# Performance work log

Measured on AMD Instinct MI355X. Metric: run time of the kernel, lower is better.

The kernel has to match this reference:

```python
import jax, jax.numpy as jnp
import numpy as np

EPS = float(np.finfo(np.float64).eps)  # np.finfo(float).eps as in torch combine


def setup_inputs() -> dict:
    key = jax.random.key(0)
    ks = jax.random.split(key, 4)
    B, E, D_in, D_h, D_out = 4096, 8, 768, 2048, 768
    return {
        "x": jax.random.normal(ks[0], (B, D_in), dtype=jnp.float32),
        "w_gate": jax.random.normal(ks[1], (D_in, E), dtype=jnp.float32) * 0.02,
        "W1": jax.random.normal(ks[2], (E, D_in, D_h), dtype=jnp.float32) * (1.0 / np.sqrt(D_in)),
        "b1": jnp.zeros((E, D_h), dtype=jnp.float32),
        "W2": jax.random.normal(ks[3], (E, D_h, D_out), dtype=jnp.float32) * (1.0 / np.sqrt(D_h)),
        "b2": jnp.zeros((E, D_out), dtype=jnp.float32),
        "k": 2,
    }


def _cv_squared(v):
    # torch .var() is unbiased (ddof=1)
    return jnp.var(v, ddof=1) / (jnp.mean(v) ** 2 + 1e-10)


def _top_k_gates(logits, k):
    B, E = logits.shape
    top_vals, top_idx = jax.lax.top_k(logits, k)        # [B, k]
    top_gates = jax.nn.softmax(top_vals, axis=1)        # softmax over the k kept logits
    gates = jnp.zeros((B, E), logits.dtype).at[jnp.arange(B)[:, None], top_idx].set(top_gates)
    return gates


def reference(x, w_gate, W1, b1, W2, b2, k):
    # --- gating (eval path: noiseless clean logits, softmax gating) ---
    logits = x @ w_gate                                  # [B, E]
    gates = _top_k_gates(logits, k)                      # [B, E], sparse (k nonzeros/row)
    # --- per-expert MLP: Linear -> gelu -> Linear -> log_softmax ---
    # Dense grouped compute over experts; gate==0 terms contribute nothing in combine.
    h = jax.nn.gelu(jnp.einsum('bi,eih->beh', x, W1) + b1[None])      # [B, E, Dh]
    lo = jax.nn.log_softmax(jnp.einsum('beh,eho->beo', h, W2) + b2[None], axis=-1)  # [B, E, Do]
    # --- combine: exp, weight by gates, scatter-add, eps-clamp, log ---
    combined = jnp.einsum('be,beo->bo', gates, jnp.exp(lo))           # [B, Do]
    y = jnp.log(jnp.where(combined == 0, EPS, combined))
    # --- load-balancing aux loss (eval: load = count of nonzero gates) ---
    importance = gates.sum(0)
    load = (gates > 0).sum(0).astype(jnp.float32)
    loss = 0.01 * (_cv_squared(importance) + _cv_squared(load))
    return y, loss
```

## Files before the change

### kernel.cpp

```cpp
#include <hip/hip_runtime.h>
#include <hip/hip_bf16.h>
#include <math.h>

typedef __hip_bfloat16 bf16;
typedef short v8s __attribute__((ext_vector_type(8)));
typedef float v4f __attribute__((ext_vector_type(4)));

#define B_TOK 4096
#define E_EXP 8
#define D_IN  768
#define D_H   2048
#define D_OUT 768
#define MAXT  72

__device__ __forceinline__ void gl_lds16(const bf16* g, bf16* l) {
  __builtin_amdgcn_global_load_lds(
      (const __attribute__((address_space(1))) unsigned int*)g,
      (__attribute__((address_space(3))) unsigned int*)l, 16, 0, 0);
}

__global__ void gate_cvt_kernel(const float* __restrict__ x, const float* __restrict__ wg,
                                bf16* __restrict__ xb,
                                float* __restrict__ gates, int* __restrict__ tidx) {
  int gt = blockIdx.x * 256 + threadIdx.x;
  int tok = gt >> 6, l = gt & 63;
  const float* xr = x + (size_t)tok * D_IN;
  bf16* xbr = xb + (size_t)tok * D_IN;
  float acc[8] = {0.f,0.f,0.f,0.f,0.f,0.f,0.f,0.f};
  #pragma unroll
  for (int i = 0; i < 3; ++i) {
    int k0 = i * 256 + l * 4;
    float4 v = *(const float4*)(xr + k0);
    union { bf16 h[4]; uint2 u; } pk;
    pk.h[0] = __float2bfloat16(v.x); pk.h[1] = __float2bfloat16(v.y);
    pk.h[2] = __float2bfloat16(v.z); pk.h[3] = __float2bfloat16(v.w);
    *(uint2*)(xbr + k0) = pk.u;
    float xv[4] = {v.x, v.y, v.z, v.w};
    #pragma unroll
    for (int j = 0; j < 4; ++j) {
      const float* wr = wg + (size_t)(k0 + j) * 8;
      float4 w0 = *(const float4*)wr;
      float4 w1 = *(const float4*)(wr + 4);
      acc[0] += xv[j] * w0.x; acc[1] += xv[j] * w0.y;
      acc[2] += xv[j] * w0.z; acc[3] += xv[j] * w0.w;
      acc[4] += xv[j] * w1.x; acc[5] += xv[j] * w1.y;
      acc[6] += xv[j] * w1.z; acc[7] += xv[j] * w1.w;
    }
  }
  #pragma unroll
  for (int d = 1; d < 64; d <<= 1)
    #pragma unroll
    for (int e = 0; e < 8; ++e) acc[e] += __shfl_xor(acc[e], d);
  if (l == 0) {
    int i1 = 0; float v1 = acc[0];
    #pragma unroll
    for (int e = 1; e < 8; ++e) if (acc[e] > v1) { v1 = acc[e]; i1 = e; }
    int i2 = -1; float v2 = -1e30f;
    #pragma unroll
    for (int e = 0; e < 8; ++e) if (e != i1 && acc[e] > v2) { v2 = acc[e]; i2 = e; }
    float ex = __expf(v2 - v1);
    float g1 = 1.f / (1.f + ex), g2 = ex / (1.f + ex);
    gates[2 * tok] = g1; gates[2 * tok + 1] = g2;
    tidx[2 * tok] = i1;  tidx[2 * tok + 1] = i2;
  }
}

__global__ void finalize_kernel(const int* __restrict__ tidx, const float* __restrict__ gates,
                                int* __restrict__ cnt_off, int* __restrict__ row_ids,
                                int* __restrict__ pos, int* __restrict__ tmap,
                                float* __restrict__ loss_out) {
  __shared__ int   hcnt[256][9];
  __shared__ float himp[256][9];
  __shared__ int   tot[8], off[8];
  __shared__ float itot[8];
  int t = threadIdx.x;
  #pragma unroll
  for (int e = 0; e < 8; ++e) { hcnt[t][e] = 0; himp[t][e] = 0.f; }
  __syncthreads();
  for (int i = 0; i < 32; ++i) {
    int idx = t * 32 + i;
    int e = tidx[idx];
    hcnt[t][e] += 1;
    himp[t][e] += gates[idx];
  }
  __syncthreads();
  if (t < 8) {
    int run = 0; float s = 0.f;
    for (int j = 0; j < 256; ++j) {
      int c = hcnt[j][t];
      hcnt[j][t] = run;
      run += c;
      s += himp[j][t];
    }
    tot[t] = run; itot[t] = s;
  }
  __syncthreads();
  if (t == 0) {
    int o = 0;
    float mi = 0.f, ml = 0.f;
    for (int e = 0; e < 8; ++e) {
      off[e] = o; o += tot[e];
      cnt_off[e] = tot[e]; cnt_off[8 + e] = off[e];
      mi += itot[e]; ml += (float)tot[e];
    }
    mi *= 0.125f; ml *= 0.125f;
    float vi = 0.f, vl = 0.f;
    for (int e = 0; e < 8; ++e) {
      float d = itot[e] - mi;        vi += d * d;
      float d2 = (float)tot[e] - ml; vl += d2 * d2;
    }
    vi /= 7.f; vl /= 7.f;
    *loss_out = 0.01f * (vi / (mi * mi + 1e-10f) + vl / (ml * ml + 1e-10f));
    int nt = 0;
    for (int e = 0; e < 8; ++e)
      for (int tt = 0; tt < (tot[e] + 127) >> 7; ++tt) {
        tmap[nt] = e; tmap[MAXT + nt] = tt; ++nt;
      }
    for (; nt < MAXT; ++nt) tmap[nt] = -1;
  }
  __syncthreads();
  for (int i = 0; i < 32; ++i) {
    int idx = t * 32 + i;
    int e = tidx[idx];
    int slot = off[e] + hcnt[t][e];
    hcnt[t][e] += 1;
    row_ids[slot] = idx >> 1;
    pos[idx] = slot;
  }
}

__global__ void transpose_cvt(const float* __restrict__ W, bf16* __restrict__ Wt,
                              int K, int N) {
  __shared__ bf16 tile[64][72];
  int e = blockIdx.z;
  int k0 = blockIdx.y * 64, n0 = blockIdx.x * 64;
  const float* Wp = W + (size_t)e * K * N;
  bf16* Wtp = Wt + (size_t)e * N * K;
  int t = threadIdx.x;
  int cr = t >> 4;
  int cc = (t & 15) * 4;
  #pragma unroll
  for (int p = 0; p < 4; ++p) {
    int kr = cr + p * 16;
    float4 v = *(const float4*)(Wp + (size_t)(k0 + kr) * N + n0 + cc);
    tile[cc + 0][kr] = __float2bfloat16(v.x);
    tile[cc + 1][kr] = __float2bfloat16(v.y);
    tile[cc + 2][kr] = __float2bfloat16(v.z);
    tile[cc + 3][kr] = __float2bfloat16(v.w);
  }
  __syncthreads();
  #pragma unroll
  for (int p = 0; p < 2; ++p) {
    int o = p * 256 + t;
    int n = o >> 3, k8 = (o & 7) * 8;
    v8s val = *(const v8s*)&tile[n][k8];
    *(v8s*)(Wtp + (size_t)(n0 + n) * K + k0 + k8) = val;
  }
}

template<int KDIM, bool GATHER, bool GELU>
__global__ __launch_bounds__(256, 2)
void gemm_mlp(const bf16* __restrict__ Ab, const bf16* __restrict__ Wt,
              const float* __restrict__ bias, bf16* __restrict__ Outb,
              const int* __restrict__ row_ids, const int* __restrict__ cnt_off,
              const int* __restrict__ tmap, const int N) {
  constexpr int BK = 64, BM = 128, BN = 128;
  constexpr int NK = KDIM / BK;
  static_assert(NK % 2 == 0 && NK >= 4, "NK even, >=4");
  __shared__ __align__(16) bf16 lds[2][(BM + BN) * BK];
  const int ti = blockIdx.y;
  const int e = tmap[ti];
  if (e < 0) return;
  const int rowb = tmap[MAXT + ti];
  const int cnt = cnt_off[e];
  const int off = cnt_off[8 + e];
  const int colb = blockIdx.x;
  const int t = (int)threadIdx.x, w = t >> 6, l = t & 63;
  const int cs = (l & 7) ^ (l >> 3);
  const bf16* gA[4];
  const bf16* gB[4];
  #pragma unroll
  for (int it = 0; it < 4; ++it) {
    int rt = (it * 4 + w) * 8 + (l >> 3);
    int r = rowb * BM + rt;
    int rc = r < cnt ? r : cnt - 1;
    long arow = GATHER ? (long)row_ids[off + rc] : (long)(off + rc);
    gA[it] = Ab + arow * (long)KDIM + cs * 8;
  }
  #pragma unroll
  for (int it = 0; it < 4; ++it) {
    int rt = (it * 4 + w) * 8 + (l >> 3);
    gB[it] = Wt + ((size_t)e * N + (size_t)colb * BN + rt) * KDIM + cs * 8;
  }
  v4f acc[4][4] = {};
  const int wm = w >> 1, wn = w & 1;

#define STAGE(b, k0) do {                                                   \
    _Pragma("unroll")                                                       \
    for (int it = 0; it < 4; ++it)                                          \
      gl_lds16(gA[it] + (k0), &lds[b][(it * 4 + w) * 512]);                 \
    _Pragma("unroll")                                                       \
    for (int it = 0; it < 4; ++it)                                          \
      gl_lds16(gB[it] + (k0), &lds[b][BM * BK + (it * 4 + w) * 512]);       \
  } while (0)

#define COMPUTE(b) do {                                                     \
    __builtin_amdgcn_s_setprio(1);                                          \
    _Pragma("unroll")                                                       \
    for (int kk = 0; kk < 2; ++kk) {                                        \
      v8s af[4], bfr[4];                                                    \
      _Pragma("unroll")                                                     \
      for (int fm = 0; fm < 4; ++fm) {                                      \
        int row = wm * 64 + fm * 16 + (l & 15);                             \
        int cg = kk * 4 + (l >> 4);                                         \
        af[fm] = *(const v8s*)(&lds[b][0] + row * BK + ((cg ^ (row & 7)) << 3)); \
      }                                                                     \
      _Pragma("unroll")                                                     \
      for (int fn = 0; fn < 4; ++fn) {                                      \
        int row = wn * 64 + fn * 16 + (l & 15);                             \
        int cg = kk * 4 + (l >> 4);                                         \
        bfr[fn] = *(const v8s*)(&lds[b][BM * BK] + row * BK + ((cg ^ (row & 7)) << 3)); \
      }                                                                     \
      _Pragma("unroll")                                                     \
      for (int fm = 0; fm < 4; ++fm)                                        \
        _Pragma("unroll")                                                   \
        for (int fn = 0; fn < 4; ++fn)                                      \
          acc[fm][fn] = __builtin_amdgcn_mfma_f32_16x16x32_bf16(af[fm], bfr[fn], acc[fm][fn], 0, 0, 0); \
    }                                                                       \
    __builtin_amdgcn_s_setprio(0);                                          \
  } while (0)

#define SB    __builtin_amdgcn_sched_barrier(0)
#define BARR  __builtin_amdgcn_s_barrier()
#define WAIT8 asm volatile("s_waitcnt vmcnt(8)" ::: "memory")
#define WAITZ asm volatile("s_waitcnt vmcnt(0)" ::: "memory")

  STAGE(0, 0);
  #pragma unroll 1
  for (int ks = 0; ks < NK - 2; ks += 2) {
    STAGE(1, (ks + 1) * BK);
    WAIT8; SB; BARR; SB;
    COMPUTE(0);
    BARR; SB;
    STAGE(0, (ks + 2) * BK);
    WAIT8; SB; BARR; SB;
    COMPUTE(1);
    BARR; SB;
  }
  STAGE(1, (NK - 1) * BK);
  WAIT8; SB; BARR; SB;
  COMPUTE(0);
  WAITZ; SB; BARR; SB;
  COMPUTE(1);
#undef STAGE
#undef COMPUTE
#undef WAIT8
#undef WAITZ

  float* eps = (float*)(&lds[0][0]) + w * (16 * 68);
  const float* bp = bias + (size_t)e * N + (size_t)colb * BN + wn * 64 + (l & 7) * 8;
  float bv[8];
  #pragma unroll
  for (int jj = 0; jj < 8; ++jj) bv[jj] = bp[jj];
  #pragma unroll
  for (int fm = 0; fm < 4; ++fm) {
    #pragma unroll
    for (int fn = 0; fn < 4; ++fn)
      #pragma unroll
      for (int q = 0; q < 4; ++q)
        eps[((l >> 4) * 4 + q) * 68 + fn * 16 + (l & 15)] = acc[fm][fn][q];
    #pragma unroll
    for (int half = 0; half < 2; ++half) {
      int row = (l >> 3) + 8 * half;
      int r = rowb * BM + wm * 64 + fm * 16 + row;
      if (r < cnt) {
        const float* rp = eps + row * 68 + (l & 7) * 8;
        union { bf16 h[8]; uint4 u; } pk;
        #pragma unroll
        for (int jj = 0; jj < 8; ++jj) {
          float v = rp[jj] + bv[jj];
          if (GELU) {
            float u = 0.7978845608028654f * (v + 0.044715f * v * v * v);
            float th = 1.f - 2.f / (__expf(2.f * u) + 1.f);
            v = 0.5f * v * (1.f + th);
          }
          pk.h[jj] = __float2bfloat16(v);
        }
        *(uint4*)(Outb + (size_t)(off + r) * N + (size_t)colb * BN + wn * 64 + (l & 7) * 8) = pk.u;
      }
    }
  }
#undef SB
#undef BARR
}

__global__ void combine_kernel(const bf16* __restrict__ z, const float* __restrict__ gates,
                               const int* __restrict__ pos, float* __restrict__ y) {
  int gt = blockIdx.x * 256 + threadIdx.x;
  int tok = gt >> 6, l = gt & 63;
  if (tok >= B_TOK) return;
  const bf16* z1 = z + (size_t)pos[2 * tok] * D_OUT;
  const bf16* z2 = z + (size_t)pos[2 * tok + 1] * D_OUT;
  float g1 = gates[2 * tok], g2 = gates[2 * tok + 1];
  float a[12], b[12];
  float m1 = -1e30f, m2 = -1e30f;
  #pragma unroll
  for (int i = 0; i < 12; ++i) {
    a[i] = __bfloat162float(z1[l + 64 * i]);
    b[i] = __bfloat162float(z2[l + 64 * i]);
    m1 = fmaxf(m1, a[i]); m2 = fmaxf(m2, b[i]);
  }
  #pragma unroll
  for (int d = 1; d < 64; d <<= 1) {
    m1 = fmaxf(m1, __shfl_xor(m1, d));
    m2 = fmaxf(m2, __shfl_xor(m2, d));
  }
  float s1 = 0.f, s2 = 0.f;
  #pragma unroll
  for (int i = 0; i < 12; ++i) { s1 += __expf(a[i] - m1); s2 += __expf(b[i] - m2); }
  #pragma unroll
  for (int d = 1; d < 64; d <<= 1) { s1 += __shfl_xor(s1, d); s2 += __shfl_xor(s2, d); }
  float c1 = g1 / s1, c2 = g2 / s2;
  #pragma unroll
  for (int i = 0; i < 12; ++i) {
    float cmb = c1 * __expf(a[i] - m1) + c2 * __expf(b[i] - m2);
    y[(size_t)tok * D_OUT + l + 64 * i] = logf(cmb == 0.f ? 2.2204460492503131e-16f : cmb);
  }
}

extern "C" void kernel_launch(void* const* d_in, const int* in_sizes, int n_in,
                              void* d_out, int out_size, void* d_ws, size_t ws_size,
                              hipStream_t stream) {
  const float* x  = (const float*)d_in[0];
  const float* wg = (const float*)d_in[1];
  const float* W1 = (const float*)d_in[2];
  const float* b1 = (const float*)d_in[3];
  const float* W2 = (const float*)d_in[4];
  const float* b2 = (const float*)d_in[5];
  float* out = (float*)d_out;

  char* ws = (char*)d_ws;
  int*   cnt_off = (int*)(ws + 0);
  float* gates   = (float*)(ws + 256);
  int*   tidx    = (int*)(ws + 256 + 32768);
  int*   pos     = (int*)(ws + 256 + 65536);
  int*   row_ids = (int*)(ws + 256 + 98304);
  int*   tmap    = (int*)(ws + 256 + 131072);
  const size_t base = 262144;
  bf16* x_bf = (bf16*)(ws + base);
  bf16* W1t  = (bf16*)(ws + base + 6291456);
  bf16* W2t  = (bf16*)(ws + base + 31457280);
  bf16* h_bf = (bf16*)(ws + base + 56623104);
  bf16* z_bf = (bf16*)(ws + base);

  transpose_cvt<<<dim3(D_H / 64,  D_IN / 64, E_EXP), 256, 0, stream>>>(W1, W1t, D_IN, D_H);
  transpose_cvt<<<dim3(D_OUT / 64, D_H / 64, E_EXP), 256, 0, stream>>>(W2, W2t, D_H, D_OUT);
  gate_cvt_kernel<<<dim3(1024), 256, 0, stream>>>(x, wg, x_bf, gates, tidx);
  finalize_kernel<<<dim3(1), 256, 0, stream>>>(tidx, gates, cnt_off, row_ids, pos, tmap,
                                               out + (size_t)B_TOK * D_OUT);
  gemm_mlp<D_IN, true,  true ><<<dim3(D_H / 128,  MAXT), 256, 0, stream>>>(
      x_bf, W1t, b1, h_bf, row_ids, cnt_off, tmap, D_H);
  gemm_mlp<D_H,  false, false><<<dim3(D_OUT / 128, MAXT), 256, 0, stream>>>(
      h_bf, W2t, b2, z_bf, row_ids, cnt_off, tmap, D_OUT);
  combine_kernel<<<dim3(1024), 256, 0, stream>>>(z_bf, gates, pos, out);
}
```

Before: 162.5 us.

## Use 256x256 GEMM tiles with 8 waves and interleaved staging in expert MLP

The grouped expert GEMMs move from 128x128 tiles with 4 waves to 256x256 tiles with 8 waves (512 threads), which halves the number of row tiles per expert and changes how the tile map is built. The K-loop now issues next-tile global-to-LDS loads partway through the MFMA work, splitting A and B staging across sub-steps, and waits on LDS reads explicitly. The second GEMM swaps its grid axes so row tiles vary fastest. Larger tiles raise data reuse per block, but they also produce fewer blocks (more idle CUs) and more padded rows for small expert groups, and they increase register and LDS pressure.

Result: no change. 164.5 us (+1.2%).

```diff
diff --git a/kernel.cpp b/kernel.cpp
--- a/kernel.cpp
+++ b/kernel.cpp
@@ -11,7 +11,7 @@
 #define D_IN  768
 #define D_H   2048
 #define D_OUT 768
-#define MAXT  72
+#define MAXT  40
 
 __device__ __forceinline__ void gl_lds16(const bf16* g, bf16* l) {
   __builtin_amdgcn_global_load_lds(
@@ -113,7 +113,7 @@
     *loss_out = 0.01f * (vi / (mi * mi + 1e-10f) + vl / (ml * ml + 1e-10f));
     int nt = 0;
     for (int e = 0; e < 8; ++e)
-      for (int tt = 0; tt < (tot[e] + 127) >> 7; ++tt) {
+      for (int tt = 0; tt < (tot[e] + 255) >> 8; ++tt) {
         tmap[nt] = e; tmap[MAXT + nt] = tt; ++nt;
       }
     for (; nt < MAXT; ++nt) tmap[nt] = -1;
@@ -158,112 +158,136 @@
   }
 }
 
-template<int KDIM, bool GATHER, bool GELU>
-__global__ __launch_bounds__(256, 2)
+template<int KDIM, bool GATHER, bool GELU, bool COLX>
+__global__ __launch_bounds__(512, 2)
 void gemm_mlp(const bf16* __restrict__ Ab, const bf16* __restrict__ Wt,
               const float* __restrict__ bias, bf16* __restrict__ Outb,
               const int* __restrict__ row_ids, const int* __restrict__ cnt_off,
               const int* __restrict__ tmap, const int N) {
-  constexpr int BK = 64, BM = 128, BN = 128;
+  constexpr int BK = 64, BM = 256, BN = 256;
   constexpr int NK = KDIM / BK;
   static_assert(NK % 2 == 0 && NK >= 4, "NK even, >=4");
   __shared__ __align__(16) bf16 lds[2][(BM + BN) * BK];
-  const int ti = blockIdx.y;
+  const int cb = COLX ? blockIdx.x : blockIdx.y;
+  const int ti = COLX ? blockIdx.y : blockIdx.x;
   const int e = tmap[ti];
   if (e < 0) return;
   const int rowb = tmap[MAXT + ti];
   const int cnt = cnt_off[e];
   const int off = cnt_off[8 + e];
-  const int colb = blockIdx.x;
   const int t = (int)threadIdx.x, w = t >> 6, l = t & 63;
   const int cs = (l & 7) ^ (l >> 3);
   const bf16* gA[4];
   const bf16* gB[4];
   #pragma unroll
   for (int it = 0; it < 4; ++it) {
-    int rt = (it * 4 + w) * 8 + (l >> 3);
+    int rt = (it * 8 + w) * 8 + (l >> 3);
     int r = rowb * BM + rt;
     int rc = r < cnt ? r : cnt - 1;
     long arow = GATHER ? (long)row_ids[off + rc] : (long)(off + rc);
     gA[it] = Ab + arow * (long)KDIM + cs * 8;
-  }
-  #pragma unroll
-  for (int it = 0; it < 4; ++it) {
-    int rt = (it * 4 + w) * 8 + (l >> 3);
-    gB[it] = Wt + ((size_t)e * N + (size_t)colb * BN + rt) * KDIM + cs * 8;
-  }
-  v4f acc[4][4] = {};
-  const int wm = w >> 1, wn = w & 1;
-
-#define STAGE(b, k0) do {                                                   \
+    gB[it] = Wt + ((size_t)e * N + (size_t)cb * BN + rt) * KDIM + cs * 8;
+  }
+  v4f acc[8][4] = {};
+  const int wm = w >> 2, wn = w & 3;
+
+#define STAGE_A(b, k0) do {                                                 \
     _Pragma("unroll")                                                       \
     for (int it = 0; it < 4; ++it)                                          \
-      gl_lds16(gA[it] + (k0), &lds[b][(it * 4 + w) * 512]);                 \
+      gl_lds16(gA[it] + (k0), &lds[b][(it * 8 + w) * 512]);                 \
+  } while (0)
+#define STAGE_B(b, k0) do {                                                 \
     _Pragma("unroll")                                                       \
     for (int it = 0; it < 4; ++it)                                          \
-      gl_lds16(gB[it] + (k0), &lds[b][BM * BK + (it * 4 + w) * 512]);       \
+      gl_lds16(gB[it] + (k0), &lds[b][BM * BK + (it * 8 + w) * 512]);       \
   } while (0)
 
-#define COMPUTE(b) do {                                                     \
-    __builtin_amdgcn_s_setprio(1);                                          \
+#define READ_A(b, fm, kk) (*(const v8s*)(&lds[b][0] +                       \
+    (wm * 128 + (fm) * 16 + (l & 15)) * 64 +                                \
+    ((((kk) * 4 + (l >> 4)) ^ (l & 7)) << 3)))
+#define READ_B(b, fn, kk) (*(const v8s*)(&lds[b][BM * BK] +                 \
+    (wn * 64 + (fn) * 16 + (l & 15)) * 64 +                                 \
+    ((((kk) * 4 + (l >> 4)) ^ (l & 7)) << 3)))
+
+#define SB    __builtin_amdgcn_sched_barrier(0)
+#define BARR  __builtin_amdgcn_s_barrier()
+#define LGKM0 asm volatile("s_waitcnt lgkmcnt(0)" ::: "memory")
+#define VM0   asm volatile("s_waitcnt vmcnt(0)" ::: "memory")
+
+#define MFMA8(fmb, fm2)                                                     \
     _Pragma("unroll")                                                       \
-    for (int kk = 0; kk < 2; ++kk) {                                        \
-      v8s af[4], bfr[4];                                                    \
+    for (int fn = 0; fn < 4; ++fn)                                          \
       _Pragma("unroll")                                                     \
-      for (int fm = 0; fm < 4; ++fm) {                                      \
-        int row = wm * 64 + fm * 16 + (l & 15);                             \
-        int cg = kk * 4 + (l >> 4);                                         \
-        af[fm] = *(const v8s*)(&lds[b][0] + row * BK + ((cg ^ (row & 7)) << 3)); \
-      }                                                                     \
+      for (int kk = 0; kk < 2; ++kk)                                        \
+        acc[(fmb) + (fm2)][fn] = __builtin_amdgcn_mfma_f32_16x16x32_bf16(   \
+            af[fm2][kk], bfr[fn][kk], acc[(fmb) + (fm2)][fn], 0, 0, 0);
+
+#define TILE(b, nb, knext) do {                                             \
+    v8s bfr[4][2];                                                          \
+    {                              \
+      v8s af[2][2];                                                         \
       _Pragma("unroll")                                                     \
       for (int fn = 0; fn < 4; ++fn) {                                      \
-        int row = wn * 64 + fn * 16 + (l & 15);                             \
-        int cg = kk * 4 + (l >> 4);                                         \
-        bfr[fn] = *(const v8s*)(&lds[b][BM * BK] + row * BK + ((cg ^ (row & 7)) << 3)); \
+        bfr[fn][0] = READ_B(b, fn, 0); bfr[fn][1] = READ_B(b, fn, 1);       \
       }                                                                     \
-      _Pragma("unroll")                                                     \
-      for (int fm = 0; fm < 4; ++fm)                                        \
-        _Pragma("unroll")                                                   \
-        for (int fn = 0; fn < 4; ++fn)                                      \
-          acc[fm][fn] = __builtin_amdgcn_mfma_f32_16x16x32_bf16(af[fm], bfr[fn], acc[fm][fn], 0, 0, 0); \
+      af[0][0] = READ_A(b, 0, 0); af[0][1] = READ_A(b, 0, 1);               \
+      af[1][0] = READ_A(b, 1, 0); af[1][1] = READ_A(b, 1, 1);               \
+      if ((knext) < KDIM) STAGE_A(nb, knext);                               \
+      LGKM0; SB;                                                            \
+      __builtin_amdgcn_s_setprio(1); MFMA8(0, 0) MFMA8(0, 1)                \
+      __builtin_amdgcn_s_setprio(0);                                        \
     }                                                                       \
-    __builtin_amdgcn_s_setprio(0);                                          \
+    {                                        \
+      v8s af[2][2];                                                         \
+      af[0][0] = READ_A(b, 2, 0); af[0][1] = READ_A(b, 2, 1);               \
+      af[1][0] = READ_A(b, 3, 0); af[1][1] = READ_A(b, 3, 1);               \
+      if ((knext) < KDIM) STAGE_B(nb, knext);                               \
+      LGKM0; SB;                                                            \
+      __builtin_amdgcn_s_setprio(1); MFMA8(2, 0) MFMA8(2, 1)                \
+      __builtin_amdgcn_s_setprio(0);                                        \
+    }                                                                       \
+    {                                                      \
+      v8s af[2][2];                                                         \
+      af[0][0] = READ_A(b, 4, 0); af[0][1] = READ_A(b, 4, 1);               \
+      af[1][0] = READ_A(b, 5, 0); af[1][1] = READ_A(b, 5, 1);               \
+      LGKM0; SB;                                                            \
+      __builtin_amdgcn_s_setprio(1); MFMA8(4, 0) MFMA8(4, 1)                \
+      __builtin_amdgcn_s_setprio(0);                                        \
+    }                                                                       \
+    {                              \
+      v8s af[2][2];                                                         \
+      af[0][0] = READ_A(b, 6, 0); af[0][1] = READ_A(b, 6, 1);               \
+      af[1][0] = READ_A(b, 7, 0); af[1][1] = READ_A(b, 7, 1);               \
+      LGKM0; SB;                                                            \
+      __builtin_amdgcn_s_setprio(1); MFMA8(6, 0) MFMA8(6, 1)                \
+      __builtin_amdgcn_s_setprio(0);                                        \
+      VM0; SB; BARR; SB;                                                    \
+    }                                                                       \
   } while (0)
 
-#define SB    __builtin_amdgcn_sched_barrier(0)
-#define BARR  __builtin_amdgcn_s_barrier()
-#define WAIT8 asm volatile("s_waitcnt vmcnt(8)" ::: "memory")
-#define WAITZ asm volatile("s_waitcnt vmcnt(0)" ::: "memory")
-
-  STAGE(0, 0);
+  STAGE_A(0, 0); STAGE_B(0, 0);
+  VM0; SB; BARR; SB;
   #pragma unroll 1
-  for (int ks = 0; ks < NK - 2; ks += 2) {
-    STAGE(1, (ks + 1) * BK);
-    WAIT8; SB; BARR; SB;
-    COMPUTE(0);
-    BARR; SB;
-    STAGE(0, (ks + 2) * BK);
-    WAIT8; SB; BARR; SB;
-    COMPUTE(1);
-    BARR; SB;
-  }
-  STAGE(1, (NK - 1) * BK);
-  WAIT8; SB; BARR; SB;
-  COMPUTE(0);
-  WAITZ; SB; BARR; SB;
-  COMPUTE(1);
-#undef STAGE
-#undef COMPUTE
-#undef WAIT8
-#undef WAITZ
+  for (int ks = 0; ks < NK; ks += 2) {
+    TILE(0, 1, (ks + 1) * BK);
+    TILE(1, 0, (ks + 2) * BK);
+  }
+#undef TILE
+#undef MFMA8
+#undef STAGE_A
+#undef STAGE_B
+#undef READ_A
+#undef READ_B
+#undef LGKM0
+#undef VM0
 
   float* eps = (float*)(&lds[0][0]) + w * (16 * 68);
-  const float* bp = bias + (size_t)e * N + (size_t)colb * BN + wn * 64 + (l & 7) * 8;
+  const float* bp = bias + (size_t)e * N + (size_t)cb * BN + wn * 64 + (l & 7) * 8;
   float bv[8];
   #pragma unroll
   for (int jj = 0; jj < 8; ++jj) bv[jj] = bp[jj];
   #pragma unroll
-  for (int fm = 0; fm < 4; ++fm) {
+  for (int fm = 0; fm < 8; ++fm) {
     #pragma unroll
     for (int fn = 0; fn < 4; ++fn)
       #pragma unroll
@@ -272,7 +296,7 @@
     #pragma unroll
     for (int half = 0; half < 2; ++half) {
       int row = (l >> 3) + 8 * half;
-      int r = rowb * BM + wm * 64 + fm * 16 + row;
+      int r = rowb * BM + wm * 128 + fm * 16 + row;
       if (r < cnt) {
         const float* rp = eps + row * 68 + (l & 7) * 8;
         union { bf16 h[8]; uint4 u; } pk;
@@ -286,7 +310,7 @@
           }
           pk.h[jj] = __float2bfloat16(v);
         }
-        *(uint4*)(Outb + (size_t)(off + r) * N + (size_t)colb * BN + wn * 64 + (l & 7) * 8) = pk.u;
+        *(uint4*)(Outb + (size_t)(off + r) * N + (size_t)cb * BN + wn * 64 + (l & 7) * 8) = pk.u;
       }
     }
   }
@@ -358,9 +382,9 @@
   gate_cvt_kernel<<<dim3(1024), 256, 0, stream>>>(x, wg, x_bf, gates, tidx);
   finalize_kernel<<<dim3(1), 256, 0, stream>>>(tidx, gates, cnt_off, row_ids, pos, tmap,
                                                out + (size_t)B_TOK * D_OUT);
-  gemm_mlp<D_IN, true,  true ><<<dim3(D_H / 128,  MAXT), 256, 0, stream>>>(
+  gemm_mlp<D_IN, true,  true,  true ><<<dim3(D_H / 256, MAXT), 512, 0, stream>>>(
       x_bf, W1t, b1, h_bf, row_ids, cnt_off, tmap, D_H);
-  gemm_mlp<D_H,  false, false><<<dim3(D_OUT / 128, MAXT), 256, 0, stream>>>(
+  gemm_mlp<D_H,  false, false, false><<<dim3(MAXT, D_OUT / 256), 512, 0, stream>>>(
       h_bf, W2t, b2, z_bf, row_ids, cnt_off, tmap, D_OUT);
   combine_kernel<<<dim3(1024), 256, 0, stream>>>(z_bf, gates, pos, out);
 }
```

## Merge prep kernels and use BK=32 GEMM with higher occupancy for second layer

Applied to the files above, without the earlier changes.

The two weight transpose/convert kernels and the gating/x-conversion kernel are merged into one launch, removing launch gaps and letting those independent jobs run at the same time. The second expert GEMM (K=2048, N=768, only 6 column tiles) switches to a new BK=32 kernel with half the LDS and launch bounds allowing 3 blocks per CU, aiming to hide latency better on this small grid. A trailing barrier is added after the last compute, since the epilogue reuses LDS. The cost is twice as many k-iterations and barriers in the second GEMM.

Result: no change. 161.2 us (-0.8%).

```diff
diff --git a/kernel.cpp b/kernel.cpp
--- a/kernel.cpp
+++ b/kernel.cpp
@@ -19,49 +19,89 @@
       (__attribute__((address_space(3))) unsigned int*)l, 16, 0, 0);
 }
 
-__global__ void gate_cvt_kernel(const float* __restrict__ x, const float* __restrict__ wg,
-                                bf16* __restrict__ xb,
-                                float* __restrict__ gates, int* __restrict__ tidx) {
-  int gt = blockIdx.x * 256 + threadIdx.x;
-  int tok = gt >> 6, l = gt & 63;
-  const float* xr = x + (size_t)tok * D_IN;
-  bf16* xbr = xb + (size_t)tok * D_IN;
-  float acc[8] = {0.f,0.f,0.f,0.f,0.f,0.f,0.f,0.f};
-  #pragma unroll
-  for (int i = 0; i < 3; ++i) {
-    int k0 = i * 256 + l * 4;
-    float4 v = *(const float4*)(xr + k0);
-    union { bf16 h[4]; uint2 u; } pk;
-    pk.h[0] = __float2bfloat16(v.x); pk.h[1] = __float2bfloat16(v.y);
-    pk.h[2] = __float2bfloat16(v.z); pk.h[3] = __float2bfloat16(v.w);
-    *(uint2*)(xbr + k0) = pk.u;
-    float xv[4] = {v.x, v.y, v.z, v.w};
-    #pragma unroll
-    for (int j = 0; j < 4; ++j) {
-      const float* wr = wg + (size_t)(k0 + j) * 8;
-      float4 w0 = *(const float4*)wr;
-      float4 w1 = *(const float4*)(wr + 4);
-      acc[0] += xv[j] * w0.x; acc[1] += xv[j] * w0.y;
-      acc[2] += xv[j] * w0.z; acc[3] += xv[j] * w0.w;
-      acc[4] += xv[j] * w1.x; acc[5] += xv[j] * w1.y;
-      acc[6] += xv[j] * w1.z; acc[7] += xv[j] * w1.w;
-    }
-  }
-  #pragma unroll
-  for (int d = 1; d < 64; d <<= 1)
-    #pragma unroll
-    for (int e = 0; e < 8; ++e) acc[e] += __shfl_xor(acc[e], d);
-  if (l == 0) {
-    int i1 = 0; float v1 = acc[0];
-    #pragma unroll
-    for (int e = 1; e < 8; ++e) if (acc[e] > v1) { v1 = acc[e]; i1 = e; }
-    int i2 = -1; float v2 = -1e30f;
-    #pragma unroll
-    for (int e = 0; e < 8; ++e) if (e != i1 && acc[e] > v2) { v2 = acc[e]; i2 = e; }
-    float ex = __expf(v2 - v1);
-    float g1 = 1.f / (1.f + ex), g2 = ex / (1.f + ex);
-    gates[2 * tok] = g1; gates[2 * tok + 1] = g2;
-    tidx[2 * tok] = i1;  tidx[2 * tok + 1] = i2;
+__global__ __launch_bounds__(256)
+void prep_kernel(const float* __restrict__ x, const float* __restrict__ wg,
+                 const float* __restrict__ W1, const float* __restrict__ W2,
+                 bf16* __restrict__ W1t, bf16* __restrict__ W2t,
+                 bf16* __restrict__ xb, float* __restrict__ gates,
+                 int* __restrict__ tidx) {
+  __shared__ bf16 tile[64][72];
+  const int b = blockIdx.x;
+  const int t = threadIdx.x;
+  if (b < 6144) {
+    const float* W; bf16* Wt; int K, N, bx, by, bz;
+    if (b < 3072) {
+      W = W1; Wt = W1t; K = D_IN; N = D_H;
+      bx = b % 32; by = (b / 32) % 12; bz = b / 384;
+    } else {
+      int c = b - 3072;
+      W = W2; Wt = W2t; K = D_H; N = D_OUT;
+      bx = c % 12; by = (c / 12) % 32; bz = c / 384;
+    }
+    int k0 = by * 64, n0 = bx * 64;
+    const float* Wp = W + (size_t)bz * K * N;
+    bf16* Wtp = Wt + (size_t)bz * N * K;
+    int cr = t >> 4;
+    int cc = (t & 15) * 4;
+    #pragma unroll
+    for (int p = 0; p < 4; ++p) {
+      int kr = cr + p * 16;
+      float4 v = *(const float4*)(Wp + (size_t)(k0 + kr) * N + n0 + cc);
+      tile[cc + 0][kr] = __float2bfloat16(v.x);
+      tile[cc + 1][kr] = __float2bfloat16(v.y);
+      tile[cc + 2][kr] = __float2bfloat16(v.z);
+      tile[cc + 3][kr] = __float2bfloat16(v.w);
+    }
+    __syncthreads();
+    #pragma unroll
+    for (int p = 0; p < 2; ++p) {
+      int o = p * 256 + t;
+      int n = o >> 3, k8 = (o & 7) * 8;
+      v8s val = *(const v8s*)&tile[n][k8];
+      *(v8s*)(Wtp + (size_t)(n0 + n) * K + k0 + k8) = val;
+    }
+  } else {
+    int gt = (b - 6144) * 256 + t;
+    int tok = gt >> 6, l = gt & 63;
+    const float* xr = x + (size_t)tok * D_IN;
+    bf16* xbr = xb + (size_t)tok * D_IN;
+    float acc[8] = {0.f,0.f,0.f,0.f,0.f,0.f,0.f,0.f};
+    #pragma unroll
+    for (int i = 0; i < 3; ++i) {
+      int k0 = i * 256 + l * 4;
+      float4 v = *(const float4*)(xr + k0);
+      union { bf16 h[4]; uint2 u; } pk;
+      pk.h[0] = __float2bfloat16(v.x); pk.h[1] = __float2bfloat16(v.y);
+      pk.h[2] = __float2bfloat16(v.z); pk.h[3] = __float2bfloat16(v.w);
+      *(uint2*)(xbr + k0) = pk.u;
+      float xv[4] = {v.x, v.y, v.z, v.w};
+      #pragma unroll
+      for (int j = 0; j < 4; ++j) {
+        const float* wr = wg + (size_t)(k0 + j) * 8;
+        float4 w0 = *(const float4*)wr;
+        float4 w1 = *(const float4*)(wr + 4);
+        acc[0] += xv[j] * w0.x; acc[1] += xv[j] * w0.y;
+        acc[2] += xv[j] * w0.z; acc[3] += xv[j] * w0.w;
+        acc[4] += xv[j] * w1.x; acc[5] += xv[j] * w1.y;
+        acc[6] += xv[j] * w1.z; acc[7] += xv[j] * w1.w;
+      }
+    }
+    #pragma unroll
+    for (int d = 1; d < 64; d <<= 1)
+      #pragma unroll
+      for (int e = 0; e < 8; ++e) acc[e] += __shfl_xor(acc[e], d);
+    if (l == 0) {
+      int i1 = 0; float v1 = acc[0];
+      #pragma unroll
+      for (int e = 1; e < 8; ++e) if (acc[e] > v1) { v1 = acc[e]; i1 = e; }
+      int i2 = -1; float v2 = -1e30f;
+      #pragma unroll
+      for (int e = 0; e < 8; ++e) if (e != i1 && acc[e] > v2) { v2 = acc[e]; i2 = e; }
+      float ex = __expf(v2 - v1);
+      float g1 = 1.f / (1.f + ex), g2 = ex / (1.f + ex);
+      gates[2 * tok] = g1; gates[2 * tok + 1] = g2;
+      tidx[2 * tok] = i1;  tidx[2 * tok + 1] = i2;
+    }
   }
 }
 
@@ -126,35 +166,6 @@
     hcnt[t][e] += 1;
     row_ids[slot] = idx >> 1;
     pos[idx] = slot;
-  }
-}
-
-__global__ void transpose_cvt(const float* __restrict__ W, bf16* __restrict__ Wt,
-                              int K, int N) {
-  __shared__ bf16 tile[64][72];
-  int e = blockIdx.z;
-  int k0 = blockIdx.y * 64, n0 = blockIdx.x * 64;
-  const float* Wp = W + (size_t)e * K * N;
-  bf16* Wtp = Wt + (size_t)e * N * K;
-  int t = threadIdx.x;
-  int cr = t >> 4;
-  int cc = (t & 15) * 4;
-  #pragma unroll
-  for (int p = 0; p < 4; ++p) {
-    int kr = cr + p * 16;
-    float4 v = *(const float4*)(Wp + (size_t)(k0 + kr) * N + n0 + cc);
-    tile[cc + 0][kr] = __float2bfloat16(v.x);
-    tile[cc + 1][kr] = __float2bfloat16(v.y);
-    tile[cc + 2][kr] = __float2bfloat16(v.z);
-    tile[cc + 3][kr] = __float2bfloat16(v.w);
-  }
-  __syncthreads();
-  #pragma unroll
-  for (int p = 0; p < 2; ++p) {
-    int o = p * 256 + t;
-    int n = o >> 3, k8 = (o & 7) * 8;
-    v8s val = *(const v8s*)&tile[n][k8];
-    *(v8s*)(Wtp + (size_t)(n0 + n) * K + k0 + k8) = val;
   }
 }
 
@@ -252,6 +263,7 @@
   COMPUTE(0);
   WAITZ; SB; BARR; SB;
   COMPUTE(1);
+  BARR; SB;
 #undef STAGE
 #undef COMPUTE
 #undef WAIT8
@@ -294,6 +306,134 @@
 #undef BARR
 }
 
+template<int KDIM, bool GELU>
+__global__ __launch_bounds__(256, 3)
+void gemm_bk32(const bf16* __restrict__ Ab, const bf16* __restrict__ Wt,
+               const float* __restrict__ bias, bf16* __restrict__ Outb,
+               const int* __restrict__ cnt_off, const int* __restrict__ tmap,
+               const int N) {
+  constexpr int BK = 32, BM = 128, BN = 128;
+  constexpr int NK = KDIM / BK;
+  static_assert(NK % 2 == 0 && NK >= 4, "NK even, >=4");
+  __shared__ __align__(16) bf16 lds[2][(BM + BN) * BK];
+  const int ti = blockIdx.y;
+  const int e = tmap[ti];
+  if (e < 0) return;
+  const int rowb = tmap[MAXT + ti];
+  const int cnt = cnt_off[e];
+  const int off = cnt_off[8 + e];
+  const int colb = blockIdx.x;
+  const int t = (int)threadIdx.x, w = t >> 6, l = t & 63;
+  const int cs = (l & 3) ^ ((l >> 3) & 3);
+  const bf16* gA[2];
+  const bf16* gB[2];
+  #pragma unroll
+  for (int it = 0; it < 2; ++it) {
+    int rt = (it * 4 + w) * 16 + (l >> 2);
+    int r = rowb * BM + rt;
+    int rc = r < cnt ? r : cnt - 1;
+    gA[it] = Ab + (long)(off + rc) * KDIM + cs * 8;
+    gB[it] = Wt + ((size_t)e * N + (size_t)colb * BN + rt) * KDIM + cs * 8;
+  }
+  v4f acc[4][4] = {};
+  const int wm = w >> 1, wn = w & 1;
+
+#define STAGE(b, k0) do {                                                   \
+    _Pragma("unroll")                                                       \
+    for (int it = 0; it < 2; ++it)                                          \
+      gl_lds16(gA[it] + (k0), &lds[b][(it * 4 + w) * 512]);                 \
+    _Pragma("unroll")                                                       \
+    for (int it = 0; it < 2; ++it)                                          \
+      gl_lds16(gB[it] + (k0), &lds[b][BM * BK + (it * 4 + w) * 512]);       \
+  } while (0)
+
+#define COMPUTE(b) do {                                                     \
+    __builtin_amdgcn_s_setprio(1);                                          \
+    v8s af[4], bfr[4];                                                      \
+    const int p = (l >> 4) ^ ((l >> 1) & 3);                                \
+    _Pragma("unroll")                                                       \
+    for (int fm = 0; fm < 4; ++fm) {                                        \
+      int row = wm * 64 + fm * 16 + (l & 15);                               \
+      af[fm] = *(const v8s*)(&lds[b][0] + row * BK + p * 8);                \
+    }                                                                       \
+    _Pragma("unroll")                                                       \
+    for (int fn = 0; fn < 4; ++fn) {                                        \
+      int row = wn * 64 + fn * 16 + (l & 15);                               \
+      bfr[fn] = *(const v8s*)(&lds[b][BM * BK] + row * BK + p * 8);         \
+    }                                                                       \
+    _Pragma("unroll")                                                       \
+    for (int fm = 0; fm < 4; ++fm)                                          \
+      _Pragma("unroll")                                                     \
+      for (int fn = 0; fn < 4; ++fn)                                        \
+        acc[fm][fn] = __builtin_amdgcn_mfma_f32_16x16x32_bf16(af[fm], bfr[fn], acc[fm][fn], 0, 0, 0); \
+    __builtin_amdgcn_s_setprio(0);                                          \
+  } while (0)
+
+#define SB    __builtin_amdgcn_sched_barrier(0)
+#define BARR  __builtin_amdgcn_s_barrier()
+#define WAIT4 asm volatile("s_waitcnt vmcnt(4)" ::: "memory")
+#define WAITZ asm volatile("s_waitcnt vmcnt(0)" ::: "memory")
+
+  STAGE(0, 0);
+  #pragma unroll 1
+  for (int ks = 0; ks < NK - 2; ks += 2) {
+    STAGE(1, (ks + 1) * BK);
+    WAIT4; SB; BARR; SB;
+    COMPUTE(0);
+    BARR; SB;
+    STAGE(0, (ks + 2) * BK);
+    WAIT4; SB; BARR; SB;
+    COMPUTE(1);
+    BARR; SB;
+  }
+  STAGE(1, (NK - 1) * BK);
+  WAIT4; SB; BARR; SB;
+  COMPUTE(0);
+  WAITZ; SB; BARR; SB;
+  COMPUTE(1);
+  BARR; SB;
+#undef STAGE
+#undef COMPUTE
+#undef WAIT4
+#undef WAITZ
+
+  float* eps = (float*)(&lds[0][0]) + w * (16 * 68);
+  const float* bp = bias + (size_t)e * N + (size_t)colb * BN + wn * 64 + (l & 7) * 8;
+  float bv[8];
+  #pragma unroll
+  for (int jj = 0; jj < 8; ++jj) bv[jj] = bp[jj];
+  #pragma unroll
+  for (int fm = 0; fm < 4; ++fm) {
+    #pragma unroll
+    for (int fn = 0; fn < 4; ++fn)
+      #pragma unroll
+      for (int q = 0; q < 4; ++q)
+        eps[((l >> 4) * 4 + q) * 68 + fn * 16 + (l & 15)] = acc[fm][fn][q];
+    #pragma unroll
+    for (int half = 0; half < 2; ++half) {
+      int row = (l >> 3) + 8 * half;
+      int r = rowb * BM + wm * 64 + fm * 16 + row;
+      if (r < cnt) {
+        const float* rp = eps + row * 68 + (l & 7) * 8;
+        union { bf16 h[8]; uint4 u; } pk;
+        #pragma unroll
+        for (int jj = 0; jj < 8; ++jj) {
+          float v = rp[jj] + bv[jj];
+          if (GELU) {
+            float u = 0.7978845608028654f * (v + 0.044715f * v * v * v);
+            float th = 1.f - 2.f / (__expf(2.f * u) + 1.f);
+            v = 0.5f * v * (1.f + th);
+          }
+          pk.h[jj] = __float2bfloat16(v);
+        }
+        *(uint4*)(Outb + (size_t)(off + r) * N + (size_t)colb * BN + wn * 64 + (l & 7) * 8) = pk.u;
+      }
+    }
+  }
+#undef SB
+#undef BARR
+}
+
 __global__ void combine_kernel(const bf16* __restrict__ z, const float* __restrict__ gates,
                                const int* __restrict__ pos, float* __restrict__ y) {
   int gt = blockIdx.x * 256 + threadIdx.x;
@@ -353,14 +493,12 @@
   bf16* h_bf = (bf16*)(ws + base + 56623104);
   bf16* z_bf = (bf16*)(ws + base);
 
-  transpose_cvt<<<dim3(D_H / 64,  D_IN / 64, E_EXP), 256, 0, stream>>>(W1, W1t, D_IN, D_H);
-  transpose_cvt<<<dim3(D_OUT / 64, D_H / 64, E_EXP), 256, 0, stream>>>(W2, W2t, D_H, D_OUT);
-  gate_cvt_kernel<<<dim3(1024), 256, 0, stream>>>(x, wg, x_bf, gates, tidx);
+  prep_kernel<<<dim3(7168), 256, 0, stream>>>(x, wg, W1, W2, W1t, W2t, x_bf, gates, tidx);
   finalize_kernel<<<dim3(1), 256, 0, stream>>>(tidx, gates, cnt_off, row_ids, pos, tmap,
                                                out + (size_t)B_TOK * D_OUT);
-  gemm_mlp<D_IN, true,  true ><<<dim3(D_H / 128,  MAXT), 256, 0, stream>>>(
+  gemm_mlp<D_IN, true, true><<<dim3(D_H / 128, MAXT), 256, 0, stream>>>(
       x_bf, W1t, b1, h_bf, row_ids, cnt_off, tmap, D_H);
-  gemm_mlp<D_H,  false, false><<<dim3(D_OUT / 128, MAXT), 256, 0, stream>>>(
-      h_bf, W2t, b2, z_bf, row_ids, cnt_off, tmap, D_OUT);
+  gemm_bk32<D_H, false><<<dim3(D_OUT / 128, MAXT), 256, 0, stream>>>(
+      h_bf, W2t, b2, z_bf, cnt_off, tmap, D_OUT);
   combine_kernel<<<dim3(1024), 256, 0, stream>>>(z_bf, gates, pos, out);
 }
```

## Merge weight transpose and gating into one prep kernel; shrink GEMM K-tile

Applied to the files above, without the earlier changes.

The two weight transpose-convert launches and the gating/x-convert launch are merged into a single prep kernel. The transpose now drops shared memory: each thread reads 32 strided floats along K and writes a contiguous 64-byte bf16 run. Separately, the grouped GEMM K-tile goes from 64 to 32 with a new LDS swizzle and launch bounds raised to 3 blocks per SM, aiming for more occupancy and less LDS per block. The cost is twice as many barrier and wait steps per K, and column-strided loads in the transpose that may coalesce less well.

Result: slower. 166.5 us (+2.4%).

```diff
diff --git a/kernel.cpp b/kernel.cpp
--- a/kernel.cpp
+++ b/kernel.cpp
@@ -19,49 +19,79 @@
       (__attribute__((address_space(3))) unsigned int*)l, 16, 0, 0);
 }
 
-__global__ void gate_cvt_kernel(const float* __restrict__ x, const float* __restrict__ wg,
-                                bf16* __restrict__ xb,
-                                float* __restrict__ gates, int* __restrict__ tidx) {
-  int gt = blockIdx.x * 256 + threadIdx.x;
-  int tok = gt >> 6, l = gt & 63;
-  const float* xr = x + (size_t)tok * D_IN;
-  bf16* xbr = xb + (size_t)tok * D_IN;
-  float acc[8] = {0.f,0.f,0.f,0.f,0.f,0.f,0.f,0.f};
-  #pragma unroll
-  for (int i = 0; i < 3; ++i) {
-    int k0 = i * 256 + l * 4;
-    float4 v = *(const float4*)(xr + k0);
-    union { bf16 h[4]; uint2 u; } pk;
-    pk.h[0] = __float2bfloat16(v.x); pk.h[1] = __float2bfloat16(v.y);
-    pk.h[2] = __float2bfloat16(v.z); pk.h[3] = __float2bfloat16(v.w);
-    *(uint2*)(xbr + k0) = pk.u;
-    float xv[4] = {v.x, v.y, v.z, v.w};
-    #pragma unroll
-    for (int j = 0; j < 4; ++j) {
-      const float* wr = wg + (size_t)(k0 + j) * 8;
-      float4 w0 = *(const float4*)wr;
-      float4 w1 = *(const float4*)(wr + 4);
-      acc[0] += xv[j] * w0.x; acc[1] += xv[j] * w0.y;
-      acc[2] += xv[j] * w0.z; acc[3] += xv[j] * w0.w;
-      acc[4] += xv[j] * w1.x; acc[5] += xv[j] * w1.y;
-      acc[6] += xv[j] * w1.z; acc[7] += xv[j] * w1.w;
-    }
-  }
-  #pragma unroll
-  for (int d = 1; d < 64; d <<= 1)
-    #pragma unroll
-    for (int e = 0; e < 8; ++e) acc[e] += __shfl_xor(acc[e], d);
-  if (l == 0) {
-    int i1 = 0; float v1 = acc[0];
-    #pragma unroll
-    for (int e = 1; e < 8; ++e) if (acc[e] > v1) { v1 = acc[e]; i1 = e; }
-    int i2 = -1; float v2 = -1e30f;
-    #pragma unroll
-    for (int e = 0; e < 8; ++e) if (e != i1 && acc[e] > v2) { v2 = acc[e]; i2 = e; }
-    float ex = __expf(v2 - v1);
-    float g1 = 1.f / (1.f + ex), g2 = ex / (1.f + ex);
-    gates[2 * tok] = g1; gates[2 * tok + 1] = g2;
-    tidx[2 * tok] = i1;  tidx[2 * tok + 1] = i2;
+__global__ __launch_bounds__(256)
+void prep_kernel(const float* __restrict__ x, const float* __restrict__ wg,
+                 const float* __restrict__ W1, const float* __restrict__ W2,
+                 bf16* __restrict__ W1t, bf16* __restrict__ W2t,
+                 bf16* __restrict__ xb, float* __restrict__ gates,
+                 int* __restrict__ tidx) {
+  const int b = blockIdx.x;
+  const int t = threadIdx.x;
+  if (b < 3072) {
+    const float* W; bf16* Wt; int K, N, kb, nb, e;
+    if (b < 1536) {
+      W = W1; Wt = W1t; K = D_IN; N = D_H;
+      e = b / 192; int rem = b % 192; kb = rem % 24; nb = rem / 24;
+    } else {
+      int c = b - 1536;
+      W = W2; Wt = W2t; K = D_H; N = D_OUT;
+      e = c / 192; int rem = c % 192; kb = rem % 64; nb = rem / 64;
+    }
+    const int w = t >> 6, l = t & 63;
+    const int k0 = kb * 32;
+    const int n  = nb * 256 + w * 64 + l;
+    const float* Wp = W + (size_t)e * K * N + (size_t)k0 * N + n;
+    float v[32];
+    #pragma unroll
+    for (int j = 0; j < 32; ++j) v[j] = Wp[(size_t)j * N];
+    union { bf16 h[32]; uint4 u[4]; } pk;
+    #pragma unroll
+    for (int j = 0; j < 32; ++j) pk.h[j] = __float2bfloat16(v[j]);
+    bf16* op = Wt + (size_t)e * N * K + (size_t)n * K + k0;
+    #pragma unroll
+    for (int s = 0; s < 4; ++s) *(uint4*)(op + s * 8) = pk.u[s];
+  } else {
+    int gt = (b - 3072) * 256 + t;
+    int tok = gt >> 6, l = gt & 63;
+    const float* xr = x + (size_t)tok * D_IN;
+    bf16* xbr = xb + (size_t)tok * D_IN;
+    float acc[8] = {0.f,0.f,0.f,0.f,0.f,0.f,0.f,0.f};
+    #pragma unroll
+    for (int i = 0; i < 3; ++i) {
+      int k0 = i * 256 + l * 4;
+      float4 v = *(const float4*)(xr + k0);
+      union { bf16 h[4]; uint2 u; } pk;
+      pk.h[0] = __float2bfloat16(v.x); pk.h[1] = __float2bfloat16(v.y);
+      pk.h[2] = __float2bfloat16(v.z); pk.h[3] = __float2bfloat16(v.w);
+      *(uint2*)(xbr + k0) = pk.u;
+      float xv[4] = {v.x, v.y, v.z, v.w};
+      #pragma unroll
+      for (int j = 0; j < 4; ++j) {
+        const float* wr = wg + (size_t)(k0 + j) * 8;
+        float4 w0 = *(const float4*)wr;
+        float4 w1 = *(const float4*)(wr + 4);
+        acc[0] += xv[j] * w0.x; acc[1] += xv[j] * w0.y;
+        acc[2] += xv[j] * w0.z; acc[3] += xv[j] * w0.w;
+        acc[4] += xv[j] * w1.x; acc[5] += xv[j] * w1.y;
+        acc[6] += xv[j] * w1.z; acc[7] += xv[j] * w1.w;
+      }
+    }
+    #pragma unroll
+    for (int d = 1; d < 64; d <<= 1)
+      #pragma unroll
+      for (int e = 0; e < 8; ++e) acc[e] += __shfl_xor(acc[e], d);
+    if (l == 0) {
+      int i1 = 0; float v1 = acc[0];
+      #pragma unroll
+      for (int e = 1; e < 8; ++e) if (acc[e] > v1) { v1 = acc[e]; i1 = e; }
+      int i2 = -1; float v2 = -1e30f;
+      #pragma unroll
+      for (int e = 0; e < 8; ++e) if (e != i1 && acc[e] > v2) { v2 = acc[e]; i2 = e; }
+      float ex = __expf(v2 - v1);
+      float g1 = 1.f / (1.f + ex), g2 = ex / (1.f + ex);
+      gates[2 * tok] = g1; gates[2 * tok + 1] = g2;
+      tidx[2 * tok] = i1;  tidx[2 * tok + 1] = i2;
+    }
   }
 }
 
@@ -129,42 +159,13 @@
   }
 }
 
-__global__ void transpose_cvt(const float* __restrict__ W, bf16* __restrict__ Wt,
-                              int K, int N) {
-  __shared__ bf16 tile[64][72];
-  int e = blockIdx.z;
-  int k0 = blockIdx.y * 64, n0 = blockIdx.x * 64;
-  const float* Wp = W + (size_t)e * K * N;
-  bf16* Wtp = Wt + (size_t)e * N * K;
-  int t = threadIdx.x;
-  int cr = t >> 4;
-  int cc = (t & 15) * 4;
-  #pragma unroll
-  for (int p = 0; p < 4; ++p) {
-    int kr = cr + p * 16;
-    float4 v = *(const float4*)(Wp + (size_t)(k0 + kr) * N + n0 + cc);
-    tile[cc + 0][kr] = __float2bfloat16(v.x);
-    tile[cc + 1][kr] = __float2bfloat16(v.y);
-    tile[cc + 2][kr] = __float2bfloat16(v.z);
-    tile[cc + 3][kr] = __float2bfloat16(v.w);
-  }
-  __syncthreads();
-  #pragma unroll
-  for (int p = 0; p < 2; ++p) {
-    int o = p * 256 + t;
-    int n = o >> 3, k8 = (o & 7) * 8;
-    v8s val = *(const v8s*)&tile[n][k8];
-    *(v8s*)(Wtp + (size_t)(n0 + n) * K + k0 + k8) = val;
-  }
-}
-
 template<int KDIM, bool GATHER, bool GELU>
-__global__ __launch_bounds__(256, 2)
-void gemm_mlp(const bf16* __restrict__ Ab, const bf16* __restrict__ Wt,
-              const float* __restrict__ bias, bf16* __restrict__ Outb,
-              const int* __restrict__ row_ids, const int* __restrict__ cnt_off,
-              const int* __restrict__ tmap, const int N) {
-  constexpr int BK = 64, BM = 128, BN = 128;
+__global__ __launch_bounds__(256, 3)
+void gemm_bk32(const bf16* __restrict__ Ab, const bf16* __restrict__ Wt,
+               const float* __restrict__ bias, bf16* __restrict__ Outb,
+               const int* __restrict__ row_ids, const int* __restrict__ cnt_off,
+               const int* __restrict__ tmap, const int N) {
+  constexpr int BK = 32, BM = 128, BN = 128;
   constexpr int NK = KDIM / BK;
   static_assert(NK % 2 == 0 && NK >= 4, "NK even, >=4");
   __shared__ __align__(16) bf16 lds[2][(BM + BN) * BK];
@@ -176,20 +177,16 @@
   const int off = cnt_off[8 + e];
   const int colb = blockIdx.x;
   const int t = (int)threadIdx.x, w = t >> 6, l = t & 63;
-  const int cs = (l & 7) ^ (l >> 3);
-  const bf16* gA[4];
-  const bf16* gB[4];
-  #pragma unroll
-  for (int it = 0; it < 4; ++it) {
-    int rt = (it * 4 + w) * 8 + (l >> 3);
+  const int cs = (l & 3) ^ ((l >> 3) & 3);
+  const bf16* gA[2];
+  const bf16* gB[2];
+  #pragma unroll
+  for (int it = 0; it < 2; ++it) {
+    int rt = (it * 4 + w) * 16 + (l >> 2);
     int r = rowb * BM + rt;
     int rc = r < cnt ? r : cnt - 1;
     long arow = GATHER ? (long)row_ids[off + rc] : (long)(off + rc);
     gA[it] = Ab + arow * (long)KDIM + cs * 8;
-  }
-  #pragma unroll
-  for (int it = 0; it < 4; ++it) {
-    int rt = (it * 4 + w) * 8 + (l >> 3);
     gB[it] = Wt + ((size_t)e * N + (size_t)colb * BN + rt) * KDIM + cs * 8;
   }
   v4f acc[4][4] = {};
@@ -197,64 +194,61 @@
 
 #define STAGE(b, k0) do {                                                   \
     _Pragma("unroll")                                                       \
-    for (int it = 0; it < 4; ++it)                                          \
+    for (int it = 0; it < 2; ++it)                                          \
       gl_lds16(gA[it] + (k0), &lds[b][(it * 4 + w) * 512]);                 \
     _Pragma("unroll")                                                       \
-    for (int it = 0; it < 4; ++it)                                          \
+    for (int it = 0; it < 2; ++it)                                          \
       gl_lds16(gB[it] + (k0), &lds[b][BM * BK + (it * 4 + w) * 512]);       \
   } while (0)
 
 #define COMPUTE(b) do {                                                     \
     __builtin_amdgcn_s_setprio(1);                                          \
-    _Pragma("unroll")                                                       \
-    for (int kk = 0; kk < 2; ++kk) {                                        \
-      v8s af[4], bfr[4];                                                    \
+    v8s af[4], bfr[4];                                                      \
+    const int p = (l >> 4) ^ ((l >> 1) & 3);                                \
+    _Pragma("unroll")                                                       \
+    for (int fm = 0; fm < 4; ++fm) {                                        \
+      int row = wm * 64 + fm * 16 + (l & 15);                               \
+      af[fm] = *(const v8s*)(&lds[b][0] + row * BK + p * 8);                \
+    }                                                                       \
+    _Pragma("unroll")                                                       \
+    for (int fn = 0; fn < 4; ++fn) {                                        \
+      int row = wn * 64 + fn * 16 + (l & 15);                               \
+      bfr[fn] = *(const v8s*)(&lds[b][BM * BK] + row * BK + p * 8);         \
+    }                                                                       \
+    _Pragma("unroll")                                                       \
+    for (int fm = 0; fm < 4; ++fm)                                          \
       _Pragma("unroll")                                                     \
-      for (int fm = 0; fm < 4; ++fm) {                                      \
-        int row = wm * 64 + fm * 16 + (l & 15);                             \
-        int cg = kk * 4 + (l >> 4);                                         \
-        af[fm] = *(const v8s*)(&lds[b][0] + row * BK + ((cg ^ (row & 7)) << 3)); \
-      }                                                                     \
-      _Pragma("unroll")                                                     \
-      for (int fn = 0; fn < 4; ++fn) {                                      \
-        int row = wn * 64 + fn * 16 + (l & 15);                             \
-        int cg = kk * 4 + (l >> 4);                                         \
-        bfr[fn] = *(const v8s*)(&lds[b][BM * BK] + row * BK + ((cg ^ (row & 7)) << 3)); \
-      }                                                                     \
-      _Pragma("unroll")                                                     \
-      for (int fm = 0; fm < 4; ++fm)                                        \
-        _Pragma("unroll")                                                   \
-        for (int fn = 0; fn < 4; ++fn)                                      \
-          acc[fm][fn] = __builtin_amdgcn_mfma_f32_16x16x32_bf16(af[fm], bfr[fn], acc[fm][fn], 0, 0, 0); \
-    }                                                                       \
+      for (int fn = 0; fn < 4; ++fn)                                        \
+        acc[fm][fn] = __builtin_amdgcn_mfma_f32_16x16x32_bf16(af[fm], bfr[fn], acc[fm][fn], 0, 0, 0); \
     __builtin_amdgcn_s_setprio(0);                                          \
   } while (0)
 
 #define SB    __builtin_amdgcn_sched_barrier(0)
 #define BARR  __builtin_amdgcn_s_barrier()
-#define WAIT8 asm volatile("s_waitcnt vmcnt(8)" ::: "memory")
+#define WAIT4 asm volatile("s_waitcnt vmcnt(4)" ::: "memory")
 #define WAITZ asm volatile("s_waitcnt vmcnt(0)" ::: "memory")
 
   STAGE(0, 0);
   #pragma unroll 1
   for (int ks = 0; ks < NK - 2; ks += 2) {
     STAGE(1, (ks + 1) * BK);
-    WAIT8; SB; BARR; SB;
+    WAIT4; SB; BARR; SB;
     COMPUTE(0);
     BARR; SB;
     STAGE(0, (ks + 2) * BK);
-    WAIT8; SB; BARR; SB;
+    WAIT4; SB; BARR; SB;
     COMPUTE(1);
     BARR; SB;
   }
   STAGE(1, (NK - 1) * BK);
-  WAIT8; SB; BARR; SB;
+  WAIT4; SB; BARR; SB;
   COMPUTE(0);
   WAITZ; SB; BARR; SB;
   COMPUTE(1);
+  BARR; SB;
 #undef STAGE
 #undef COMPUTE
-#undef WAIT8
+#undef WAIT4
 #undef WAITZ
 
   float* eps = (float*)(&lds[0][0]) + w * (16 * 68);
@@ -353,14 +347,12 @@
   bf16* h_bf = (bf16*)(ws + base + 56623104);
   bf16* z_bf = (bf16*)(ws + base);
 
-  transpose_cvt<<<dim3(D_H / 64,  D_IN / 64, E_EXP), 256, 0, stream>>>(W1, W1t, D_IN, D_H);
-  transpose_cvt<<<dim3(D_OUT / 64, D_H / 64, E_EXP), 256, 0, stream>>>(W2, W2t, D_H, D_OUT);
-  gate_cvt_kernel<<<dim3(1024), 256, 0, stream>>>(x, wg, x_bf, gates, tidx);
+  prep_kernel<<<dim3(4096), 256, 0, stream>>>(x, wg, W1, W2, W1t, W2t, x_bf, gates, tidx);
   finalize_kernel<<<dim3(1), 256, 0, stream>>>(tidx, gates, cnt_off, row_ids, pos, tmap,
                                                out + (size_t)B_TOK * D_OUT);
-  gemm_mlp<D_IN, true,  true ><<<dim3(D_H / 128,  MAXT), 256, 0, stream>>>(
+  gemm_bk32<D_IN, true,  true ><<<dim3(D_H / 128, MAXT), 256, 0, stream>>>(
       x_bf, W1t, b1, h_bf, row_ids, cnt_off, tmap, D_H);
-  gemm_mlp<D_H,  false, false><<<dim3(D_OUT / 128, MAXT), 256, 0, stream>>>(
+  gemm_bk32<D_H,  false, false><<<dim3(D_OUT / 128, MAXT), 256, 0, stream>>>(
       h_bf, W2t, b2, z_bf, row_ids, cnt_off, tmap, D_OUT);
   combine_kernel<<<dim3(1024), 256, 0, stream>>>(z_bf, gates, pos, out);
 }
```
